# Kernel tuning notes

Measured on AMD Instinct MI355X. Metric: run time of the kernel, lower is better.

Reference implementation:

```python
import jax, jax.numpy as jnp
import numpy as np

B = 2048          # puzzles
E_PER = 1620      # 81 cells * 20 constraint neighbors
N = B * 81        # total nodes
NFEAT = 10


def _winit(key, fan_in, fan_out):
    s = (1.0 / np.sqrt(fan_in)).astype(np.float32) if isinstance(fan_in, np.ndarray) else 1.0 / np.sqrt(fan_in)
    return jax.random.uniform(key, (fan_in, fan_out), jnp.float32, -s, s)


def setup_inputs() -> dict:
    key = jax.random.key(0)
    ks = jax.random.split(key, 20)
    x = jax.random.normal(ks[0], (N, NFEAT), jnp.float32)
    # batched edge index [B, 2, E_PER]; values are global node ids
    edge_index = jax.random.randint(ks[1], (B, 2, E_PER), 0, N, dtype=jnp.int32)
    dims = [(NFEAT, 16), (16, 32), (32, 64), (64, 32), (32, 16)]
    params = {}
    for i, (ci, co) in enumerate(dims, start=1):
        params[f'W{i}'] = _winit(ks[2 * i], ci, co)
        params[f'b{i}'] = jnp.zeros((co,), jnp.float32)
    params['fW1'] = _winit(ks[14], 16, 16)
    params['fb1'] = jnp.zeros((16,), jnp.float32)
    params['fW2'] = _winit(ks[15], 16, 9)
    params['fb2'] = jnp.zeros((9,), jnp.float32)
    return {'x': x, 'edge_index': edge_index, **params}


def _gcn(h, W, b, src, dst, norm):
    # GCNConv: out[i] = sum_{j->i} norm_ij * (h_j W) + b   (self-loops included in src/dst)
    h = h @ W                                  # [N, Cout] small GEMM
    msg = h[src] * norm[:, None]               # gather + scale, [E+N, Cout]
    return jax.ops.segment_sum(msg, dst, num_segments=N) + b


def reference(x, edge_index, W1, b1, W2, b2, W3, b3, W4, b4, W5, b5, fW1, fb1, fW2, fb2):
    # replicate edge_index.permute(1,2,0).reshape(2,-1)
    ei = jnp.transpose(edge_index, (1, 2, 0)).reshape(2, -1)
    src, dst = ei[0], ei[1]
    # add self loops (PyG gcn_norm default)
    loop = jnp.arange(N, dtype=src.dtype)
    src = jnp.concatenate([src, loop])
    dst = jnp.concatenate([dst, loop])
    deg = jax.ops.segment_sum(jnp.ones(src.shape, x.dtype), dst, num_segments=N)
    dinv = jnp.where(deg > 0, jax.lax.rsqrt(jnp.maximum(deg, 1e-12)), 0.0)
    norm = dinv[src] * dinv[dst]               # shared across layers (same graph)
    h = jax.nn.relu(_gcn(x, W1, b1, src, dst, norm))
    h = jax.nn.relu(_gcn(h, W2, b2, src, dst, norm))
    h = jax.nn.relu(_gcn(h, W3, b3, src, dst, norm))
    h = jax.nn.relu(_gcn(h, W4, b4, src, dst, norm))
    h = jax.nn.relu(_gcn(h, W5, b5, src, dst, norm))
    h = h.reshape(-1, 16)
    h = jax.nn.relu(h @ fW1 + fb1)
    h = h @ fW2 + fb2
    return h.reshape(-1, 81, 9)
```

## Files before the change

### kernel.cpp

```cpp
#include <hip/hip_runtime.h>


#define NN    165888
#define NBAT  2048
#define EPER  1620
#define NEDGE (NBAT * EPER)
#define ETOT  (NEDGE + NN)
#define NBKT  648
#define NBLK  512
#define SLICE 20736


__device__ inline void blk_scan256(int val, int& excl, int& total, int* sw) {
  int lane = threadIdx.x & 63, w = threadIdx.x >> 6;
  int x = val;
#pragma unroll
  for (int off = 1; off < 64; off <<= 1) {
    int y = __shfl_up(x, off);
    if (lane >= off) x += y;
  }
  if (lane == 63) sw[w] = x;
  __syncthreads();
  int woff = 0;
  if (w > 0) woff = sw[0];
  if (w > 1) woff += sw[1];
  if (w > 2) woff += sw[2];
  total = sw[0] + sw[1] + sw[2] + sw[3];
  excl = woff + x - val;
}


__global__ __launch_bounds__(256) void k_count(const int* __restrict__ ei,
                                               int* __restrict__ counts) {
  __shared__ int cnt[NBKT];
  int t = threadIdx.x;
  for (int k = t; k < NBKT; k += 256) cnt[k] = 0;
  __syncthreads();
  int b0 = blockIdx.x * 4;
  for (int b = b0; b < b0 + 4; ++b) {
    const int* dstp = ei + (size_t)b * (2 * EPER) + EPER;
    for (int e = t; e < EPER; e += 256) atomicAdd(&cnt[dstp[e] >> 8], 1);
  }
  __syncthreads();
  for (int k = t; k < NBKT; k += 256) counts[blockIdx.x * NBKT + k] = cnt[k];
}

__global__ __launch_bounds__(256) void k_scan(const int* __restrict__ counts,
                                              int* __restrict__ basesT,
                                              int* __restrict__ btot) {
  int bkt = blockIdx.x, t = threadIdx.x;
  int a = counts[(2 * t)     * NBKT + bkt];
  int b = counts[(2 * t + 1) * NBKT + bkt];
  __shared__ int sw[4];
  int excl, tot;
  blk_scan256(a + b, excl, tot, sw);
  basesT[bkt * NBLK + 2 * t]     = excl;
  basesT[bkt * NBLK + 2 * t + 1] = excl + a;
  if (t == 255) btot[bkt] = tot;
}

__global__ __launch_bounds__(1024) void k_pscan(const int* __restrict__ btot,
                                                int* __restrict__ pbase) {
  __shared__ int s[NBKT];
  int t = threadIdx.x;
  if (t < NBKT) s[t] = btot[t];
  __syncthreads();
  for (int off = 1; off < NBKT; off <<= 1) {
    int v = (t < NBKT && t >= off) ? s[t - off] : 0;
    __syncthreads();
    if (t < NBKT) s[t] += v;
    __syncthreads();
  }
  if (t < NBKT) pbase[t + 1] = s[t];
  if (t == 0)   pbase[0] = 0;
}

__global__ __launch_bounds__(256) void k_scat(const int* __restrict__ ei,
                                              const int* __restrict__ basesT,
                                              const int* __restrict__ pbase,
                                              unsigned int* __restrict__ pairs) {
  __shared__ int cur[NBKT];
  int t = threadIdx.x;
  for (int k = t; k < NBKT; k += 256)
    cur[k] = pbase[k] + basesT[k * NBLK + blockIdx.x];
  __syncthreads();
  int b0 = blockIdx.x * 4;
  for (int b = b0; b < b0 + 4; ++b) {
    const int* srcp = ei + (size_t)b * (2 * EPER);
    const int* dstp = srcp + EPER;
    for (int e = t; e < EPER; e += 256) {
      int d = dstp[e];
      unsigned int s = (unsigned int)srcp[e];
      int pos = atomicAdd(&cur[d >> 8], 1);
      pairs[pos] = s | ((unsigned int)(d & 255) << 24);
    }
  }
}

__global__ __launch_bounds__(256) void k_build(const unsigned int* __restrict__ pairs,
                                               const int* __restrict__ pbase,
                                               const float* __restrict__ x,
                                               const float* __restrict__ W1,
                                               int* __restrict__ row_start,
                                               int* __restrict__ row_end,
                                               float* __restrict__ dinv,
                                               int* __restrict__ csr,
                                               float* __restrict__ g0) {
  __shared__ int cnt[256];
  __shared__ int sw[4];
  __shared__ float sW[160];
  int bkt = blockIdx.x, t = threadIdx.x;
  cnt[t] = 0;
  if (t < 160) sW[t] = W1[t];
  __syncthreads();
  int p0 = pbase[bkt], p1 = pbase[bkt + 1];
  for (int k = p0 + t; k < p1; k += 256)
    atomicAdd(&cnt[pairs[k] >> 24], 1);
  __syncthreads();
  int indeg = cnt[t];
  int excl, tot;
  blk_scan256(indeg, excl, tot, sw);
  int csrbase = p0 + bkt * 256;
  int rs   = csrbase + excl + t;
  int node = bkt * 256 + t;
  int d    = indeg + 1;
  float di = rsqrtf((float)d);
  row_start[node] = rs;
  row_end[node]   = rs + d;
  dinv[node] = di;
  csr[rs] = node;
  __syncthreads();
  cnt[t] = rs + 1;
  __syncthreads();
  for (int k = p0 + t; k < p1; k += 256) {
    unsigned int pr = pairs[k];
    int pos = atomicAdd(&cnt[pr >> 24], 1);
    csr[pos] = (int)(pr & 0x00FFFFFFu);
  }
  float r[10];
#pragma unroll
  for (int k = 0; k < 10; ++k) r[k] = x[(size_t)node * 10 + k];
  float acc[16];
#pragma unroll
  for (int j = 0; j < 16; ++j) acc[j] = 0.0f;
#pragma unroll
  for (int k = 0; k < 10; ++k) {
    float rv = r[k];
#pragma unroll
    for (int j = 0; j < 16; ++j) acc[j] = fmaf(rv, sW[k * 16 + j], acc[j]);
  }
  float* op = g0 + (size_t)node * 16;
#pragma unroll
  for (int j = 0; j < 16; j += 4)
    *(float4*)(op + j) = make_float4(acc[j] * di, acc[j+1] * di,
                                     acc[j+2] * di, acc[j+3] * di);
}


template <int C, int EPI>
__device__ inline float4 agg_core(const float* __restrict__ g,
                                  const int* __restrict__ csr,
                                  int rs, int re, int q, int gl) {
  constexpr int LG = C / 4;
  float4 acc = make_float4(0.f, 0.f, 0.f, 0.f);
  const float* gq = g + (size_t)q * 4;
  int iters = 0;
  for (int p = rs; p < re; p += EPI) {
    ++iters;
    int m[EPI / LG];
#pragma unroll
    for (int u = 0; u < EPI / LG; ++u) {
      int idx = p + u * LG + q;
      m[u] = csr[idx < re ? idx : re - 1];
    }
    float4 v[EPI];
#pragma unroll
    for (int j = 0; j < EPI; ++j) {
      int s = __shfl(m[j / LG], gl + (j % LG));
      v[j] = *(const float4*)(gq + (size_t)s * C);
    }
#pragma unroll
    for (int j = 0; j < EPI; ++j) {
      acc.x += v[j].x; acc.y += v[j].y; acc.z += v[j].z; acc.w += v[j].w;
    }
  }
  float dups = (float)(iters * EPI - (re - rs));
  int slast = csr[re - 1];
  float4 vl = *(const float4*)(gq + (size_t)slast * C);
  acc.x = fmaf(-dups, vl.x, acc.x);
  acc.y = fmaf(-dups, vl.y, acc.y);
  acc.z = fmaf(-dups, vl.z, acc.z);
  acc.w = fmaf(-dups, vl.w, acc.w);
  return acc;
}


__global__ __launch_bounds__(256) void k_agg_ep16(const float* __restrict__ g,
                                                  const int* __restrict__ row_start,
                                                  const int* __restrict__ row_end,
                                                  const int* __restrict__ csr,
                                                  const float* __restrict__ dinv,
                                                  const float* __restrict__ bias,
                                                  float* __restrict__ out) {
  constexpr int LG = 4, NPB = 64, SPB = SLICE / NPB;
  int t  = threadIdx.x;
  int q  = t & (LG - 1);
  int bi = blockIdx.x;
  int vb = (bi & 7) * SPB + (bi >> 3);
  int i  = vb * NPB + t / LG;
  int gl = (t & 63) & ~(LG - 1);
  float4 acc = agg_core<16, 16>(g, csr, row_start[i], row_end[i], q, gl);
  float di = dinv[i];
  float4 bb = *(const float4*)(bias + q * 4);
  acc.x = fmaxf(fmaf(di, acc.x, bb.x), 0.f) * di;
  acc.y = fmaxf(fmaf(di, acc.y, bb.y), 0.f) * di;
  acc.z = fmaxf(fmaf(di, acc.z, bb.z), 0.f) * di;
  acc.w = fmaxf(fmaf(di, acc.w, bb.w), 0.f) * di;
  *(float4*)(out + (size_t)i * 16 + q * 4) = acc;
}


__global__ __launch_bounds__(256) void k_agg_g2(const float* __restrict__ g,
                                                const int* __restrict__ row_start,
                                                const int* __restrict__ row_end,
                                                const int* __restrict__ csr,
                                                const float* __restrict__ dinv,
                                                const float* __restrict__ W2,
                                                const float* __restrict__ b2,
                                                float* __restrict__ out) {
  constexpr int CI = 16, CO = 32, LG = 4, NPB = 64, SPB = SLICE / NPB, RP = 20;
  __shared__ float sW[CI * CO];
  __shared__ float sB[CO];
  __shared__ float rows[NPB * RP];
  __shared__ float sdi[NPB];
  int t = threadIdx.x;
  for (int k = t; k < CI * CO; k += 256) sW[k] = W2[k];
  if (t < CO) sB[t] = b2[t];
  int bi = blockIdx.x;
  int vb = (bi & 7) * SPB + (bi >> 3);
  int nbase = vb * NPB;
  int q = t & (LG - 1), nl = t / LG;
  int i = nbase + nl;
  int gl = (t & 63) & ~(LG - 1);
  float4 acc = agg_core<16, 16>(g, csr, row_start[i], row_end[i], q, gl);
  float di = dinv[i];
  acc.x *= di; acc.y *= di; acc.z *= di; acc.w *= di;
  *(float4*)&rows[nl * RP + q * 4] = acc;
  if (q == 0) sdi[nl] = di;
  __syncthreads();
  int n2 = t >> 2, c = t & 3;
  float o[8];
#pragma unroll
  for (int j = 0; j < 8; ++j) o[j] = sB[c * 8 + j];
  const float* row = &rows[n2 * RP];
#pragma unroll
  for (int k = 0; k < CI; ++k) {
    float rv = row[k];
#pragma unroll
    for (int j = 0; j < 8; ++j) o[j] = fmaf(rv, sW[k * CO + c * 8 + j], o[j]);
  }
  float d2 = sdi[n2];
#pragma unroll
  for (int j = 0; j < 8; ++j) o[j] = fmaxf(o[j], 0.f) * d2;
  float* op = out + (size_t)(nbase + n2) * CO + c * 8;
  *(float4*)op       = make_float4(o[0], o[1], o[2], o[3]);
  *(float4*)(op + 4) = make_float4(o[4], o[5], o[6], o[7]);
}


__global__ __launch_bounds__(256) void k_agg_g34(const float* __restrict__ g,
                                                 const int* __restrict__ row_start,
                                                 const int* __restrict__ row_end,
                                                 const int* __restrict__ csr,
                                                 const float* __restrict__ dinv,
                                                 const float* __restrict__ W3,
                                                 const float* __restrict__ b3,
                                                 const float* __restrict__ W4,
                                                 float* __restrict__ out) {
  constexpr int LG = 8, NPB = 32, SPB = SLICE / NPB, RP = 36, HP = 68;
  __shared__ float sW3[32 * 64];
  __shared__ float sW4[64 * 32];
  __shared__ float sB3[64];
  __shared__ float rows[NPB * RP];
  __shared__ float hrows[NPB * HP];
  __shared__ float sdi[NPB];
  int t = threadIdx.x;
  for (int k = t; k < 2048; k += 256) { sW3[k] = W3[k]; sW4[k] = W4[k]; }
  if (t < 64) sB3[t] = b3[t];
  int bi = blockIdx.x;
  int vb = (bi & 7) * SPB + (bi >> 3);
  int nbase = vb * NPB;
  int q = t & (LG - 1), nl = t / LG;
  int i = nbase + nl;
  int gl = (t & 63) & ~(LG - 1);
  float4 acc = agg_core<32, 8>(g, csr, row_start[i], row_end[i], q, gl);
  float di = dinv[i];
  acc.x *= di; acc.y *= di; acc.z *= di; acc.w *= di;
  *(float4*)&rows[nl * RP + q * 4] = acc;
  if (q == 0) sdi[nl] = di;
  __syncthreads();
  int n2 = t >> 3, c = t & 7;
  {
    float o[8];
#pragma unroll
    for (int j = 0; j < 8; ++j) o[j] = sB3[c * 8 + j];
    const float* row = &rows[n2 * RP];
#pragma unroll
    for (int k = 0; k < 32; ++k) {
      float rv = row[k];
#pragma unroll
      for (int j = 0; j < 8; ++j) o[j] = fmaf(rv, sW3[k * 64 + c * 8 + j], o[j]);
    }
    float* hp = &hrows[n2 * HP + c * 8];
#pragma unroll
    for (int j = 0; j < 8; ++j) hp[j] = fmaxf(o[j], 0.f);
  }
  __syncthreads();
  {
    float o[4] = {0.f, 0.f, 0.f, 0.f};
    const float* hp = &hrows[n2 * HP];
#pragma unroll
    for (int k = 0; k < 64; ++k) {
      float hv = hp[k];
#pragma unroll
      for (int j = 0; j < 4; ++j) o[j] = fmaf(hv, sW4[k * 32 + c * 4 + j], o[j]);
    }
    float d2 = sdi[n2];
#pragma unroll
    for (int j = 0; j < 4; ++j) o[j] *= d2;
    *(float4*)(out + (size_t)(nbase + n2) * 32 + c * 4)
        = make_float4(o[0], o[1], o[2], o[3]);
  }
}


__global__ __launch_bounds__(256) void k_agg_g5(const float* __restrict__ g,
                                                const int* __restrict__ row_start,
                                                const int* __restrict__ row_end,
                                                const int* __restrict__ csr,
                                                const float* __restrict__ dinv,
                                                const float* __restrict__ b4,
                                                const float* __restrict__ W5,
                                                float* __restrict__ out) {
  constexpr int LG = 8, NPB = 32, SPB = SLICE / NPB, RP = 36;
  __shared__ float sW[32 * 16];
  __shared__ float rows[NPB * RP];
  __shared__ float sdi[NPB];
  int t = threadIdx.x;
  for (int k = t; k < 512; k += 256) sW[k] = W5[k];
  int bi = blockIdx.x;
  int vb = (bi & 7) * SPB + (bi >> 3);
  int nbase = vb * NPB;
  int q = t & (LG - 1), nl = t / LG;
  int i = nbase + nl;
  int gl = (t & 63) & ~(LG - 1);
  float4 acc = agg_core<32, 16>(g, csr, row_start[i], row_end[i], q, gl);
  float di = dinv[i];
  float4 bb = *(const float4*)(b4 + q * 4);
  acc.x = fmaxf(fmaf(di, acc.x, bb.x), 0.f);
  acc.y = fmaxf(fmaf(di, acc.y, bb.y), 0.f);
  acc.z = fmaxf(fmaf(di, acc.z, bb.z), 0.f);
  acc.w = fmaxf(fmaf(di, acc.w, bb.w), 0.f);
  *(float4*)&rows[nl * RP + q * 4] = acc;
  if (q == 0) sdi[nl] = di;
  __syncthreads();
  int n2 = t >> 3, c = t & 7;
  float o0 = 0.f, o1 = 0.f;
  const float* row = &rows[n2 * RP];
#pragma unroll
  for (int k = 0; k < 32; ++k) {
    float rv = row[k];
    o0 = fmaf(rv, sW[k * 16 + c * 2],     o0);
    o1 = fmaf(rv, sW[k * 16 + c * 2 + 1], o1);
  }
  float d2 = sdi[n2];
  *(float2*)(out + (size_t)(nbase + n2) * 16 + c * 2) = make_float2(o0 * d2, o1 * d2);
}


__global__ __launch_bounds__(256) void k_agg_mlp(const float* __restrict__ g,
                                                 const int* __restrict__ row_start,
                                                 const int* __restrict__ row_end,
                                                 const int* __restrict__ csr,
                                                 const float* __restrict__ dinv,
                                                 const float* __restrict__ b5,
                                                 const float* __restrict__ fW1,
                                                 const float* __restrict__ fb1,
                                                 const float* __restrict__ fW2,
                                                 const float* __restrict__ fb2,
                                                 float* __restrict__ out) {
  constexpr int LG = 4, NPB = 64, SPB = SLICE / NPB, RP = 20;
  __shared__ float sW1[256], sW2[144], sB1[16], sB2[9];
  __shared__ float rows[NPB * RP];
  __shared__ float zrows[NPB * RP];
  __shared__ float ost[NPB * 9];
  int t = threadIdx.x;
  sW1[t] = fW1[t];
  if (t < 144) sW2[t] = fW2[t];
  if (t < 16)  sB1[t] = fb1[t];
  if (t < 9)   sB2[t] = fb2[t];
  int bi = blockIdx.x;
  int vb = (bi & 7) * SPB + (bi >> 3);
  int nbase = vb * NPB;
  int q = t & (LG - 1), nl = t / LG;
  int i = nbase + nl;
  int gl = (t & 63) & ~(LG - 1);
  float4 acc = agg_core<16, 16>(g, csr, row_start[i], row_end[i], q, gl);
  float di = dinv[i];
  float4 bb = *(const float4*)(b5 + q * 4);
  acc.x = fmaxf(fmaf(di, acc.x, bb.x), 0.f);
  acc.y = fmaxf(fmaf(di, acc.y, bb.y), 0.f);
  acc.z = fmaxf(fmaf(di, acc.z, bb.z), 0.f);
  acc.w = fmaxf(fmaf(di, acc.w, bb.w), 0.f);
  *(float4*)&rows[nl * RP + q * 4] = acc;
  __syncthreads();
  int n2 = t >> 2, c = t & 3;
  {
    float o[4];
#pragma unroll
    for (int j = 0; j < 4; ++j) o[j] = sB1[c * 4 + j];
    const float* row = &rows[n2 * RP];
#pragma unroll
    for (int k = 0; k < 16; ++k) {
      float rv = row[k];
#pragma unroll
      for (int j = 0; j < 4; ++j) o[j] = fmaf(rv, sW1[k * 16 + c * 4 + j], o[j]);
    }
    float* zp = &zrows[n2 * RP + c * 4];
#pragma unroll
    for (int j = 0; j < 4; ++j) zp[j] = fmaxf(o[j], 0.f);
  }
  __syncthreads();
  if (c < 3) {
    float o[3];
#pragma unroll
    for (int j = 0; j < 3; ++j) o[j] = sB2[c * 3 + j];
    const float* zp = &zrows[n2 * RP];
#pragma unroll
    for (int k = 0; k < 16; ++k) {
      float zv = zp[k];
#pragma unroll
      for (int j = 0; j < 3; ++j) o[j] = fmaf(zv, sW2[k * 9 + c * 3 + j], o[j]);
    }
#pragma unroll
    for (int j = 0; j < 3; ++j) ost[n2 * 9 + c * 3 + j] = o[j];
  }
  __syncthreads();
  float* ob = out + (size_t)nbase * 9;
  for (int k = t; k < NPB * 9; k += 256) ob[k] = ost[k];
}


extern "C" void kernel_launch(void* const* d_in, const int* in_sizes, int n_in,
                              void* d_out, int out_size, void* d_ws, size_t ws_size,
                              hipStream_t stream) {
  const float* x   = (const float*)d_in[0];
  const int*   ei  = (const int*)d_in[1];
  const float* W1  = (const float*)d_in[2];
  const float* b1  = (const float*)d_in[3];
  const float* W2  = (const float*)d_in[4];
  const float* b2  = (const float*)d_in[5];
  const float* W3  = (const float*)d_in[6];
  const float* b3  = (const float*)d_in[7];
  const float* W4  = (const float*)d_in[8];
  const float* b4  = (const float*)d_in[9];
  const float* W5  = (const float*)d_in[10];
  const float* b5  = (const float*)d_in[11];
  const float* fW1 = (const float*)d_in[12];
  const float* fb1 = (const float*)d_in[13];
  const float* fW2 = (const float*)d_in[14];
  const float* fb2 = (const float*)d_in[15];
  float* out = (float*)d_out;

  char* ws = (char*)d_ws;
  size_t off = 0;
  auto alloc = [&](size_t bytes) -> char* {
    char* p = ws + off;
    off += (bytes + 255) & ~(size_t)255;
    return p;
  };
  int*   counts  = (int*)  alloc((size_t)NBLK * NBKT * 4);
  int*   basesT  = (int*)  alloc((size_t)NBKT * NBLK * 4);
  int*   btot    = (int*)  alloc((size_t)NBKT * 4);
  int*   pbase   = (int*)  alloc((size_t)(NBKT + 1) * 4);
  unsigned int* pairs = (unsigned int*)alloc((size_t)NEDGE * 4);
  int*   rs_     = (int*)  alloc((size_t)NN * 4);
  int*   re_     = (int*)  alloc((size_t)NN * 4);
  float* dinv    = (float*)alloc((size_t)NN * 4);
  int*   csr     = (int*)  alloc((size_t)ETOT * 4);
  float* P16a    = (float*)alloc((size_t)NN * 16 * 4);
  float* P16b    = (float*)alloc((size_t)NN * 16 * 4);
  float* P32a    = (float*)alloc((size_t)NN * 32 * 4);
  float* P32b    = (float*)alloc((size_t)NN * 32 * 4);

  k_count<<<NBLK, 256, 0, stream>>>(ei, counts);
  k_scan <<<NBKT, 256, 0, stream>>>(counts, basesT, btot);
  k_pscan<<<1, 1024, 0, stream>>>(btot, pbase);
  k_scat <<<NBLK, 256, 0, stream>>>(ei, basesT, pbase, pairs);
  k_build<<<NBKT, 256, 0, stream>>>(pairs, pbase, x, W1, rs_, re_, dinv, csr, P16a);

  k_agg_ep16<<<NN / 64, 256, 0, stream>>>(P16a, rs_, re_, csr, dinv, b1, P16b);
  k_agg_g2<<<NN / 64, 256, 0, stream>>>(P16b, rs_, re_, csr, dinv, W2, b2, P32a);
  k_agg_g34<<<NN / 32, 256, 0, stream>>>(P32a, rs_, re_, csr, dinv, W3, b3, W4, P32b);
  k_agg_g5<<<NN / 32, 256, 0, stream>>>(P32b, rs_, re_, csr, dinv, b4, W5, P16a);
  k_agg_mlp<<<NN / 64, 256, 0, stream>>>(P16a, rs_, re_, csr, dinv, b5,
                                         fW1, fb1, fW2, fb2, out);
}
```

Baseline: 455.3 us.

## Fold bucket prefix scan into scatter/build kernels and cache pairs in LDS

```diff
diff --git a/kernel.cpp b/kernel.cpp
--- a/kernel.cpp
+++ b/kernel.cpp
@@ -9,6 +9,7 @@
 #define NBKT  648
 #define NBLK  512
 #define SLICE 20736
+#define BCAP  6144
 
 
 __device__ inline void blk_scan256(int val, int& excl, int& total, int* sw) {
@@ -27,6 +28,23 @@
   if (w > 2) woff += sw[2];
   total = sw[0] + sw[1] + sw[2] + sw[3];
   excl = woff + x - val;
+}
+
+__device__ inline void pbase_scan(const int* __restrict__ btot, int* pb, int* sw) {
+  int t = threadIdx.x;
+  int e0 = 0, e1 = 0, e2 = 0, s = 0;
+  if (t < 216) {
+    e0 = btot[3 * t]; e1 = btot[3 * t + 1]; e2 = btot[3 * t + 2];
+    s = e0 + e1 + e2;
+  }
+  int excl, tot;
+  blk_scan256(s, excl, tot, sw);
+  if (t < 216) {
+    pb[3 * t]     = excl;
+    pb[3 * t + 1] = excl + e0;
+    pb[3 * t + 2] = excl + e0 + e1;
+  }
+  __syncthreads();
 }
 
 
@@ -59,30 +77,17 @@
   if (t == 255) btot[bkt] = tot;
 }
 
-__global__ __launch_bounds__(1024) void k_pscan(const int* __restrict__ btot,
-                                                int* __restrict__ pbase) {
-  __shared__ int s[NBKT];
-  int t = threadIdx.x;
-  if (t < NBKT) s[t] = btot[t];
-  __syncthreads();
-  for (int off = 1; off < NBKT; off <<= 1) {
-    int v = (t < NBKT && t >= off) ? s[t - off] : 0;
-    __syncthreads();
-    if (t < NBKT) s[t] += v;
-    __syncthreads();
-  }
-  if (t < NBKT) pbase[t + 1] = s[t];
-  if (t == 0)   pbase[0] = 0;
-}
-
 __global__ __launch_bounds__(256) void k_scat(const int* __restrict__ ei,
                                               const int* __restrict__ basesT,
-                                              const int* __restrict__ pbase,
+                                              const int* __restrict__ btot,
                                               unsigned int* __restrict__ pairs) {
   __shared__ int cur[NBKT];
+  __shared__ int pb[NBKT];
+  __shared__ int sw[4];
+  pbase_scan(btot, pb, sw);
   int t = threadIdx.x;
   for (int k = t; k < NBKT; k += 256)
-    cur[k] = pbase[k] + basesT[k * NBLK + blockIdx.x];
+    cur[k] = pb[k] + basesT[k * NBLK + blockIdx.x];
   __syncthreads();
   int b0 = blockIdx.x * 4;
   for (int b = b0; b < b0 + 4; ++b) {
@@ -98,7 +103,7 @@
 }
 
 __global__ __launch_bounds__(256) void k_build(const unsigned int* __restrict__ pairs,
-                                               const int* __restrict__ pbase,
+                                               const int* __restrict__ btot,
                                                const float* __restrict__ x,
                                                const float* __restrict__ W1,
                                                int* __restrict__ row_start,
@@ -106,16 +111,22 @@
                                                float* __restrict__ dinv,
                                                int* __restrict__ csr,
                                                float* __restrict__ g0) {
+  __shared__ int pb[NBKT];
+  __shared__ int sw[4];
   __shared__ int cnt[256];
-  __shared__ int sw[4];
+  __shared__ unsigned int sp[BCAP];
   __shared__ float sW[160];
   int bkt = blockIdx.x, t = threadIdx.x;
   cnt[t] = 0;
   if (t < 160) sW[t] = W1[t];
-  __syncthreads();
-  int p0 = pbase[bkt], p1 = pbase[bkt + 1];
-  for (int k = p0 + t; k < p1; k += 256)
-    atomicAdd(&cnt[pairs[k] >> 24], 1);
+  pbase_scan(btot, pb, sw);
+  int p0 = pb[bkt];
+  int n  = btot[bkt];
+  for (int k = t; k < n; k += 256) {
+    unsigned int pr = pairs[p0 + k];
+    if (k < BCAP) sp[k] = pr;
+    atomicAdd(&cnt[pr >> 24], 1);
+  }
   __syncthreads();
   int indeg = cnt[t];
   int excl, tot;
@@ -132,8 +143,8 @@
   __syncthreads();
   cnt[t] = rs + 1;
   __syncthreads();
-  for (int k = p0 + t; k < p1; k += 256) {
-    unsigned int pr = pairs[k];
+  for (int k = t; k < n; k += 256) {
+    unsigned int pr = (k < BCAP) ? sp[k] : pairs[p0 + k];
     int pos = atomicAdd(&cnt[pr >> 24], 1);
     csr[pos] = (int)(pr & 0x00FFFFFFu);
   }
@@ -354,7 +365,7 @@
   int q = t & (LG - 1), nl = t / LG;
   int i = nbase + nl;
   int gl = (t & 63) & ~(LG - 1);
-  float4 acc = agg_core<32, 16>(g, csr, row_start[i], row_end[i], q, gl);
+  float4 acc = agg_core<32, 8>(g, csr, row_start[i], row_end[i], q, gl);
   float di = dinv[i];
   float4 bb = *(const float4*)(b4 + q * 4);
   acc.x = fmaxf(fmaf(di, acc.x, bb.x), 0.f);
@@ -482,7 +493,6 @@
   int*   counts  = (int*)  alloc((size_t)NBLK * NBKT * 4);
   int*   basesT  = (int*)  alloc((size_t)NBKT * NBLK * 4);
   int*   btot    = (int*)  alloc((size_t)NBKT * 4);
-  int*   pbase   = (int*)  alloc((size_t)(NBKT + 1) * 4);
   unsigned int* pairs = (unsigned int*)alloc((size_t)NEDGE * 4);
   int*   rs_     = (int*)  alloc((size_t)NN * 4);
   int*   re_     = (int*)  alloc((size_t)NN * 4);
@@ -495,9 +505,8 @@
 
   k_count<<<NBLK, 256, 0, stream>>>(ei, counts);
   k_scan <<<NBKT, 256, 0, stream>>>(counts, basesT, btot);
-  k_pscan<<<1, 1024, 0, stream>>>(btot, pbase);
-  k_scat <<<NBLK, 256, 0, stream>>>(ei, basesT, pbase, pairs);
-  k_build<<<NBKT, 256, 0, stream>>>(pairs, pbase, x, W1, rs_, re_, dinv, csr, P16a);
+  k_scat <<<NBLK, 256, 0, stream>>>(ei, basesT, btot, pairs);
+  k_build<<<NBKT, 256, 0, stream>>>(pairs, btot, x, W1, rs_, re_, dinv, csr, P16a);
 
   k_agg_ep16<<<NN / 64, 256, 0, stream>>>(P16a, rs_, re_, csr, dinv, b1, P16b);
   k_agg_g2<<<NN / 64, 256, 0, stream>>>(P16b, rs_, re_, csr, dinv, W2, b2, P32a);
```

Result: slower. 472.0 us (+3.6%).
